# Kernel optimization log

Measured on AMD Instinct MI355X. Metric: run time of the kernel, lower is better.

## Reference

```python
import jax, jax.numpy as jnp
import numpy as np

B, S, IN, H = 64, 1024, 256, 512

def setup_inputs() -> dict:
    key = jax.random.key(0)
    ks = jax.random.split(key, 9)
    inputs = jax.random.normal(ks[0], (B, S, IN), dtype=jnp.float32)
    timestamps = jax.random.uniform(ks[1], (B, S), dtype=jnp.float32)
    input_lens = jax.random.randint(ks[2], (B,), 1, S + 1, dtype=jnp.int64)
    sc_h = 1.0 / np.sqrt(H)
    sc_i = 1.0 / np.sqrt(IN)
    # torch Linear: y = x @ W.T + b; store transposed weights [in, out]
    W_all = jax.random.uniform(ks[3], (H, 4 * H), jnp.float32, -sc_h, sc_h)
    b_all = jax.random.uniform(ks[4], (4 * H,), jnp.float32, -sc_h, sc_h)
    U_all = jax.random.uniform(ks[5], (IN, 4 * H), jnp.float32, -sc_i, sc_i)
    b_u = jax.random.uniform(ks[6], (4 * H,), jnp.float32, -sc_i, sc_i)
    W_d = jax.random.uniform(ks[7], (H, H), jnp.float32, -sc_h, sc_h)
    b_d = jax.random.uniform(ks[8], (H,), jnp.float32, -sc_h, sc_h)
    return {"inputs": inputs, "timestamps": timestamps, "input_lens": input_lens,
            "W_all": W_all, "b_all": b_all, "U_all": U_all, "b_u": b_u,
            "W_d": W_d, "b_d": b_d}

def _time_lstm(inputs, timestamps, input_lens, W_all, b_all, U_all, b_u, W_d, b_d):
    b = inputs.shape[0]
    hdim = W_d.shape[0]
    # precompute input projection once: [B,S,4H]
    x_proj = jnp.einsum('bsi,ig->bsg', inputs, U_all) + b_u
    # elapse gate: 1 / log(e + dt), [B,S,1]
    g = 1.0 / jnp.log(jnp.float32(np.e) + timestamps)

    def step(carry, xs):
        h, c = carry
        x_t, g_t = xs  # [B,4H], [B]
        c_s1 = jnp.tanh(c @ W_d + b_d)
        c_adj = c - c_s1 + c_s1 * g_t[:, None]
        outs = h @ W_all + b_all + x_t
        f, i, o, c_tmp = jnp.split(outs, 4, axis=1)
        c_new = jax.nn.sigmoid(f) * c_adj + jax.nn.sigmoid(i) * jnp.tanh(c_tmp)
        h_new = jax.nn.sigmoid(o) * jnp.tanh(c_new)
        return (h_new, c_new), (h_new, c_new)

    h0 = jnp.zeros((b, hdim), inputs.dtype)
    c0 = jnp.zeros((b, hdim), inputs.dtype)
    xs = (jnp.swapaxes(x_proj, 0, 1), jnp.swapaxes(g, 0, 1))  # time-major
    _, (h_seq, c_seq) = jax.lax.scan(step, (h0, c0), xs)
    h_seq = jnp.swapaxes(h_seq, 0, 1)  # [B,S,H]
    c_seq = jnp.swapaxes(c_seq, 0, 1)

    seq = inputs.shape[1]
    mask = (jnp.arange(seq)[None, :] < input_lens[:, None])  # [B,S]
    outputs = jnp.where(mask[:, :, None], h_seq, 0.0)  # zeros past length, like original
    last_idx = (input_lens - 1)[:, None, None]  # [B,1,1]
    last_h = jnp.take_along_axis(h_seq, jnp.broadcast_to(last_idx, (b, 1, hdim)), axis=1)[:, 0]
    last_c = jnp.take_along_axis(c_seq, jnp.broadcast_to(last_idx, (b, 1, hdim)), axis=1)[:, 0]
    return outputs, last_h, last_c

def reference(inputs, timestamps, input_lens, W_all, b_all, U_all, b_u, W_d, b_d):
    return _time_lstm(inputs, timestamps, input_lens, W_all, b_all, U_all, b_u, W_d, b_d)
```

## Files before the change

kernel.cpp:

```cpp
#include <hip/hip_runtime.h>


typedef _Float16 f16;
typedef _Float16 f16x8 __attribute__((ext_vector_type(8)));
typedef float f32x4 __attribute__((ext_vector_type(4)));

#define S_ 1024
#define IN_ 256
#define H_ 512
#define ECONST 2.718281828459045f

__device__ __forceinline__ float sigf(float x) { return 1.0f / (1.0f + __expf(-x)); }
__device__ __forceinline__ float tanh_f(float x) { return 1.0f - 2.0f / (__expf(2.0f * x) + 1.0f); }

__device__ __forceinline__ unsigned int pack_hc(float h, float c) {
    union { f16 f; unsigned short u; } ph, pc;
    ph.f = (f16)h; pc.f = (f16)c;
    return ((unsigned int)pc.u << 16) | (unsigned int)ph.u;
}

__launch_bounds__(320, 2)
__global__ void tlstm_scan(
    const float* __restrict__ inputs, const float* __restrict__ tstamps,
    const int* __restrict__ lens,
    const float* __restrict__ W_all, const float* __restrict__ b_all,
    const float* __restrict__ U_all, const float* __restrict__ b_u,
    const float* __restrict__ W_d, const float* __restrict__ b_d,
    float* __restrict__ out0, float* __restrict__ out1, float* __restrict__ out2,
    unsigned long long* __restrict__ hcbuf, unsigned int* __restrict__ flags)
{
    __shared__ __align__(16) f16 A_sm[96 * 16 * 8];
    __shared__ __align__(16) f16 C_sm[64 * 16 * 8];
    __shared__ float outs_sm[5 * 16 * 17];
    __shared__ float c_loc[16 * 16];
    __shared__ float bias_sm[5 * 16];
    __shared__ int   len_sm[16];

    const int tid    = threadIdx.x;
    const int grp    = blockIdx.x & 3;
    const int member = blockIdx.x >> 2;
    const int wave   = tid >> 6;
    const int lane   = tid & 63;
    const int q      = lane >> 4;
    const int r16    = lane & 15;
    const int j0     = member * 16;

    f16x8 bw[24];
    if (wave < 4) {
        const int col = wave * 512 + j0 + r16;
#pragma unroll
        for (int kk = 0; kk < 24; ++kk) {
            f16x8 v;
            const int kbase = kk * 32 + q * 8;
#pragma unroll
            for (int e = 0; e < 8; ++e) {
                const int k = kbase + e;
                const float w = (kk < 16) ? W_all[k * 2048 + col]
                                          : U_all[(k - 512) * 2048 + col];
                v[e] = (f16)w;
            }
            bw[kk] = v;
        }
    } else {
        const int col = j0 + r16;
#pragma unroll
        for (int kk = 0; kk < 16; ++kk) {
            f16x8 v;
            const int kbase = kk * 32 + q * 8;
#pragma unroll
            for (int e = 0; e < 8; ++e) v[e] = (f16)W_d[(kbase + e) * 512 + col];
            bw[kk] = v;
        }
#pragma unroll
        for (int kk = 16; kk < 24; ++kk) bw[kk] = bw[0];
    }

    int sl[7];
    int ns = 0;
    for (int s = wave; s < 32; s += 5)
        if (s != member) sl[ns++] = s;

    {
        uint4 z; z.x = z.y = z.z = z.w = 0u;
        uint4* a4 = (uint4*)A_sm;
        uint4* c4 = (uint4*)C_sm;
        for (int i = tid; i < 1024; i += 320) { a4[i] = z; c4[i] = z; }
        if (tid < 256) c_loc[tid] = 0.0f;
        if (tid < 64) {
            const int w = tid >> 4, n = tid & 15;
            const int col = w * 512 + j0 + n;
            bias_sm[w * 16 + n] = b_all[col] + b_u[col];
        } else if (tid < 80) {
            const int n = tid & 15;
            bias_sm[64 + n] = b_d[j0 + n];
        }
        if (tid < 16) len_sm[tid] = lens[grp * 16 + tid];
        for (int idx = tid; idx < 1024; idx += 320) {
            const int b = idx >> 6;
            const int kx0 = (idx & 63) << 2;
            const float4 v = *(const float4*)&inputs[(((size_t)(grp * 16 + b)) * S_ + 0) * IN_ + kx0];
            union { f16 h[4]; uint2 u; } p;
            p.h[0] = (f16)v.x; p.h[1] = (f16)v.y; p.h[2] = (f16)v.z; p.h[3] = (f16)v.w;
            const int kb = 64 + (kx0 >> 3), e = kx0 & 7;
            *(uint2*)&A_sm[(kb * 16 + b) * 8 + e] = p.u;
        }
    }
    __syncthreads();

    unsigned long long* const hc_g = hcbuf + (size_t)grp * 2 * 4096;
    unsigned int* const flg = flags + grp * 32;

    for (int t = 0; t < S_; ++t) {
        float ts = 0.0f;
        if (tid < 256) {
            const int gb = grp * 16 + (tid >> 4);
            ts = tstamps[(size_t)gb * S_ + t];
        }

        f32x4 acc0 = {0.f, 0.f, 0.f, 0.f}, acc1 = {0.f, 0.f, 0.f, 0.f};
        if (wave < 4) {
            const f16* abase = &A_sm[(q * 16 + r16) * 8];
#pragma unroll
            for (int kk = 0; kk < 24; ++kk) {
                const f16x8 a = *(const f16x8*)(abase + kk * 512);
                if (kk & 1) acc1 = __builtin_amdgcn_mfma_f32_16x16x32_f16(a, bw[kk], acc1, 0, 0, 0);
                else        acc0 = __builtin_amdgcn_mfma_f32_16x16x32_f16(a, bw[kk], acc0, 0, 0, 0);
            }
        } else {
            const f16* abase = &C_sm[(q * 16 + r16) * 8];
#pragma unroll
            for (int kk = 0; kk < 16; ++kk) {
                const f16x8 a = *(const f16x8*)(abase + kk * 512);
                if (kk & 1) acc1 = __builtin_amdgcn_mfma_f32_16x16x32_f16(a, bw[kk], acc1, 0, 0, 0);
                else        acc0 = __builtin_amdgcn_mfma_f32_16x16x32_f16(a, bw[kk], acc0, 0, 0, 0);
            }
        }
        const f32x4 acc = acc0 + acc1;
#pragma unroll
        for (int r = 0; r < 4; ++r)
            outs_sm[(wave * 16 + q * 4 + r) * 17 + r16] = acc[r];
        __syncthreads();

        if (tid < 256) {
            const int b = tid >> 4, jj = tid & 15;
            const int gb = grp * 16 + b;
            const float f  = outs_sm[(0 * 16 + b) * 17 + jj] + bias_sm[0  + jj];
            const float i_ = outs_sm[(1 * 16 + b) * 17 + jj] + bias_sm[16 + jj];
            const float o  = outs_sm[(2 * 16 + b) * 17 + jj] + bias_sm[32 + jj];
            const float ct = outs_sm[(3 * 16 + b) * 17 + jj] + bias_sm[48 + jj];
            const float d  = outs_sm[(4 * 16 + b) * 17 + jj] + bias_sm[64 + jj];
            const float gt = 1.0f / __logf(ECONST + ts);
            const float cs1   = tanh_f(d);
            const float cprev = c_loc[tid];
            const float cadj  = cprev - cs1 + cs1 * gt;
            const float cnew  = sigf(f) * cadj + sigf(i_) * tanh_f(ct);
            const float hnew  = sigf(o) * tanh_f(cnew);
            c_loc[tid] = cnew;
            const int col = j0 + jj;
            const int len = len_sm[b];
            out0[((size_t)gb * S_ + t) * H_ + col] = (t < len) ? hnew : 0.0f;
            if (t == len - 1) {
                out1[gb * H_ + col] = hnew;
                out2[gb * H_ + col] = cnew;
            }
            const int fi = ((col >> 3) * 16 + b) * 8 + (col & 7);
            ((f16*)A_sm)[fi] = (f16)hnew;
            ((f16*)C_sm)[fi] = (f16)cnew;
            unsigned int* dw = (unsigned int*)(hc_g + (size_t)(t & 1) * 4096);
            __hip_atomic_store(dw + member * 256 + tid, pack_hc(hnew, cnew),
                               __ATOMIC_RELAXED, __HIP_MEMORY_SCOPE_AGENT);
        }
        __syncthreads();

        if (t < S_ - 1) {
            const unsigned int tag = (unsigned int)(t + 1);
            if (tid == 0)
                __hip_atomic_store(&flg[member], tag,
                                   __ATOMIC_RELAXED, __HIP_MEMORY_SCOPE_AGENT);

            float4 xv[4];
            if (tid < 256) {
#pragma unroll
                for (int k2 = 0; k2 < 4; ++k2) {
                    const int idx = k2 * 256 + tid;
                    const int b = idx >> 6;
                    const int kx0 = (idx & 63) << 2;
                    xv[k2] = *(const float4*)&inputs[(((size_t)(grp * 16 + b)) * S_ + (t + 1)) * IN_ + kx0];
                }
            }

            for (;;) {
                unsigned int fl = tag;
                if (lane < ns)
                    fl = __hip_atomic_load(&flg[sl[lane]],
                                           __ATOMIC_RELAXED, __HIP_MEMORY_SCOPE_AGENT);
                if (__ballot(fl >= tag) == ~0ull) break;
            }

            const unsigned long long* src = hc_g + (size_t)(t & 1) * 4096;
            unsigned long long v[7][2];
#pragma unroll
            for (int u = 0; u < 7; ++u) {
                if (u < ns) {
                    const int s = sl[u];
                    v[u][0] = __hip_atomic_load(src + s * 128 + lane,
                                                __ATOMIC_RELAXED, __HIP_MEMORY_SCOPE_AGENT);
                    v[u][1] = __hip_atomic_load(src + s * 128 + 64 + lane,
                                                __ATOMIC_RELAXED, __HIP_MEMORY_SCOPE_AGENT);
                }
            }
#pragma unroll
            for (int u = 0; u < 7; ++u) {
                if (u < ns) {
                    const int s = sl[u];
#pragma unroll
                    for (int dd = 0; dd < 2; ++dd) {
                        const int j = dd * 64 + lane;
                        const int b = j >> 3;
                        const int colL = (j & 7) * 2;
                        const int col = s * 16 + colL;
                        const unsigned long long qv = v[u][dd];
                        const unsigned int d0 = (unsigned int)qv;
                        const unsigned int d1 = (unsigned int)(qv >> 32);
                        const unsigned int hpair = (d0 & 0xFFFFu) | (d1 << 16);
                        const unsigned int cpair = (d0 >> 16) | (d1 & 0xFFFF0000u);
                        const int fi = ((col >> 3) * 16 + b) * 8 + (col & 7);
                        *(unsigned int*)((f16*)A_sm + fi) = hpair;
                        *(unsigned int*)((f16*)C_sm + fi) = cpair;
                    }
                }
            }

            if (tid < 256) {
#pragma unroll
                for (int k2 = 0; k2 < 4; ++k2) {
                    const int idx = k2 * 256 + tid;
                    const int b = idx >> 6;
                    const int kx0 = (idx & 63) << 2;
                    union { f16 h[4]; uint2 u; } p;
                    p.h[0] = (f16)xv[k2].x; p.h[1] = (f16)xv[k2].y;
                    p.h[2] = (f16)xv[k2].z; p.h[3] = (f16)xv[k2].w;
                    const int kb = 64 + (kx0 >> 3), e = kx0 & 7;
                    *(uint2*)&A_sm[(kb * 16 + b) * 8 + e] = p.u;
                }
            }
            __syncthreads();
        }
    }
}

extern "C" void kernel_launch(void* const* d_in, const int* in_sizes, int n_in,
                              void* d_out, int out_size, void* d_ws, size_t ws_size,
                              hipStream_t stream) {
    const float* inputs  = (const float*)d_in[0];
    const float* tstamps = (const float*)d_in[1];
    const int*   lens    = (const int*)d_in[2];
    const float* W_all   = (const float*)d_in[3];
    const float* b_all   = (const float*)d_in[4];
    const float* U_all   = (const float*)d_in[5];
    const float* b_u     = (const float*)d_in[6];
    const float* W_d     = (const float*)d_in[7];
    const float* b_d     = (const float*)d_in[8];

    float* out0 = (float*)d_out;
    float* out1 = out0 + (size_t)64 * 1024 * 512;
    float* out2 = out1 + (size_t)64 * 512;

    char* ws = (char*)d_ws;
    unsigned int* flags = (unsigned int*)ws;
    unsigned long long* hcbuf = (unsigned long long*)(ws + 1024);

    hipMemsetAsync(ws, 0, 1024, stream);

    tlstm_scan<<<dim3(128), dim3(320), 0, stream>>>(
        inputs, tstamps, lens, W_all, b_all, U_all, b_u, W_d, b_d,
        out0, out1, out2, hcbuf, flags);
}
```

Before: 3.488 ms.

## Replace flag-based barrier with tagged per-element h/c exchange polling

Drops the separate per-block flag array and its store/poll handshake. Each h and c value is now written as a 32-bit word holding the step tag in its upper 16 bits, and consumers poll the data itself until every tag matches. This removes one global round trip and one __syncthreads per step, at the cost of doubling the exchanged bytes and having each of 256 threads poll 64 words. Every block now reads the full buffer, including its own slice, rather than only other members' slices. The memset is removed and launch bounds are relaxed to one block per SM; stale workspace contents could in principle alias a tag.

```diff
diff --git a/kernel.cpp b/kernel.cpp
--- a/kernel.cpp
+++ b/kernel.cpp
@@ -13,13 +13,11 @@
 __device__ __forceinline__ float sigf(float x) { return 1.0f / (1.0f + __expf(-x)); }
 __device__ __forceinline__ float tanh_f(float x) { return 1.0f - 2.0f / (__expf(2.0f * x) + 1.0f); }
 
-__device__ __forceinline__ unsigned int pack_hc(float h, float c) {
-    union { f16 f; unsigned short u; } ph, pc;
-    ph.f = (f16)h; pc.f = (f16)c;
-    return ((unsigned int)pc.u << 16) | (unsigned int)ph.u;
+__device__ __forceinline__ unsigned short f16bits(float x) {
+    union { f16 f; unsigned short u; } p; p.f = (f16)x; return p.u;
 }
 
-__launch_bounds__(320, 2)
+__launch_bounds__(320, 1)
 __global__ void tlstm_scan(
     const float* __restrict__ inputs, const float* __restrict__ tstamps,
     const int* __restrict__ lens,
@@ -27,7 +25,7 @@
     const float* __restrict__ U_all, const float* __restrict__ b_u,
     const float* __restrict__ W_d, const float* __restrict__ b_d,
     float* __restrict__ out0, float* __restrict__ out1, float* __restrict__ out2,
-    unsigned long long* __restrict__ hcbuf, unsigned int* __restrict__ flags)
+    unsigned int* __restrict__ hbuf, unsigned int* __restrict__ cbuf)
 {
     __shared__ __align__(16) f16 A_sm[96 * 16 * 8];
     __shared__ __align__(16) f16 C_sm[64 * 16 * 8];
@@ -74,11 +72,6 @@
 #pragma unroll
         for (int kk = 16; kk < 24; ++kk) bw[kk] = bw[0];
     }
-
-    int sl[7];
-    int ns = 0;
-    for (int s = wave; s < 32; s += 5)
-        if (s != member) sl[ns++] = s;
 
     {
         uint4 z; z.x = z.y = z.z = z.w = 0u;
@@ -91,31 +84,26 @@
             const int col = w * 512 + j0 + n;
             bias_sm[w * 16 + n] = b_all[col] + b_u[col];
         } else if (tid < 80) {
-            const int n = tid & 15;
-            bias_sm[64 + n] = b_d[j0 + n];
+            bias_sm[64 + (tid & 15)] = b_d[j0 + (tid & 15)];
         }
         if (tid < 16) len_sm[tid] = lens[grp * 16 + tid];
         for (int idx = tid; idx < 1024; idx += 320) {
             const int b = idx >> 6;
             const int kx0 = (idx & 63) << 2;
-            const float4 v = *(const float4*)&inputs[(((size_t)(grp * 16 + b)) * S_ + 0) * IN_ + kx0];
+            const float4 v = *(const float4*)&inputs[(((size_t)(grp * 16 + b)) * S_) * IN_ + kx0];
             union { f16 h[4]; uint2 u; } p;
             p.h[0] = (f16)v.x; p.h[1] = (f16)v.y; p.h[2] = (f16)v.z; p.h[3] = (f16)v.w;
-            const int kb = 64 + (kx0 >> 3), e = kx0 & 7;
-            *(uint2*)&A_sm[(kb * 16 + b) * 8 + e] = p.u;
+            *(uint2*)&A_sm[((64 + (kx0 >> 3)) * 16 + b) * 8 + (kx0 & 7)] = p.u;
         }
     }
     __syncthreads();
 
-    unsigned long long* const hc_g = hcbuf + (size_t)grp * 2 * 4096;
-    unsigned int* const flg = flags + grp * 32;
+    unsigned int* const hb_g = hbuf + (size_t)grp * 16384;
+    unsigned int* const cb_g = cbuf + (size_t)grp * 16384;
 
     for (int t = 0; t < S_; ++t) {
         float ts = 0.0f;
-        if (tid < 256) {
-            const int gb = grp * 16 + (tid >> 4);
-            ts = tstamps[(size_t)gb * S_ + t];
-        }
+        if (tid < 256) ts = tstamps[(size_t)(grp * 16 + (tid >> 4)) * S_ + t];
 
         f32x4 acc0 = {0.f, 0.f, 0.f, 0.f}, acc1 = {0.f, 0.f, 0.f, 0.f};
         if (wave < 4) {
@@ -140,6 +128,10 @@
         for (int r = 0; r < 4; ++r)
             outs_sm[(wave * 16 + q * 4 + r) * 17 + r16] = acc[r];
         __syncthreads();
+
+        const unsigned int tag = (unsigned int)(t + 1);
+        unsigned int* const hph = hb_g + (t & 1) * 8192;
+        unsigned int* const cph = cb_g + (t & 1) * 8192;
 
         if (tid < 256) {
             const int b = tid >> 4, jj = tid & 15;
@@ -163,21 +155,16 @@
                 out1[gb * H_ + col] = hnew;
                 out2[gb * H_ + col] = cnew;
             }
-            const int fi = ((col >> 3) * 16 + b) * 8 + (col & 7);
-            ((f16*)A_sm)[fi] = (f16)hnew;
-            ((f16*)C_sm)[fi] = (f16)cnew;
-            unsigned int* dw = (unsigned int*)(hc_g + (size_t)(t & 1) * 4096);
-            __hip_atomic_store(dw + member * 256 + tid, pack_hc(hnew, cnew),
-                               __ATOMIC_RELAXED, __HIP_MEMORY_SCOPE_AGENT);
-        }
-        __syncthreads();
+            if (t < S_ - 1) {
+                const int ci = member * 256 + tid;
+                __hip_atomic_store(hph + ci, (tag << 16) | (unsigned int)f16bits(hnew),
+                                   __ATOMIC_RELAXED, __HIP_MEMORY_SCOPE_AGENT);
+                __hip_atomic_store(cph + ci, (tag << 16) | (unsigned int)f16bits(cnew),
+                                   __ATOMIC_RELAXED, __HIP_MEMORY_SCOPE_AGENT);
+            }
+        }
 
         if (t < S_ - 1) {
-            const unsigned int tag = (unsigned int)(t + 1);
-            if (tid == 0)
-                __hip_atomic_store(&flg[member], tag,
-                                   __ATOMIC_RELAXED, __HIP_MEMORY_SCOPE_AGENT);
-
             float4 xv[4];
             if (tid < 256) {
 #pragma unroll
@@ -185,53 +172,49 @@
                     const int idx = k2 * 256 + tid;
                     const int b = idx >> 6;
                     const int kx0 = (idx & 63) << 2;
-                    xv[k2] = *(const float4*)&inputs[(((size_t)(grp * 16 + b)) * S_ + (t + 1)) * IN_ + kx0];
-                }
-            }
-
-            for (;;) {
-                unsigned int fl = tag;
-                if (lane < ns)
-                    fl = __hip_atomic_load(&flg[sl[lane]],
-                                           __ATOMIC_RELAXED, __HIP_MEMORY_SCOPE_AGENT);
-                if (__ballot(fl >= tag) == ~0ull) break;
-            }
-
-            const unsigned long long* src = hc_g + (size_t)(t & 1) * 4096;
-            unsigned long long v[7][2];
-#pragma unroll
-            for (int u = 0; u < 7; ++u) {
-                if (u < ns) {
-                    const int s = sl[u];
-                    v[u][0] = __hip_atomic_load(src + s * 128 + lane,
-                                                __ATOMIC_RELAXED, __HIP_MEMORY_SCOPE_AGENT);
-                    v[u][1] = __hip_atomic_load(src + s * 128 + 64 + lane,
-                                                __ATOMIC_RELAXED, __HIP_MEMORY_SCOPE_AGENT);
-                }
-            }
-#pragma unroll
-            for (int u = 0; u < 7; ++u) {
-                if (u < ns) {
-                    const int s = sl[u];
-#pragma unroll
-                    for (int dd = 0; dd < 2; ++dd) {
-                        const int j = dd * 64 + lane;
-                        const int b = j >> 3;
-                        const int colL = (j & 7) * 2;
-                        const int col = s * 16 + colL;
-                        const unsigned long long qv = v[u][dd];
-                        const unsigned int d0 = (unsigned int)qv;
-                        const unsigned int d1 = (unsigned int)(qv >> 32);
-                        const unsigned int hpair = (d0 & 0xFFFFu) | (d1 << 16);
-                        const unsigned int cpair = (d0 >> 16) | (d1 & 0xFFFF0000u);
-                        const int fi = ((col >> 3) * 16 + b) * 8 + (col & 7);
-                        *(unsigned int*)((f16*)A_sm + fi) = hpair;
-                        *(unsigned int*)((f16*)C_sm + fi) = cpair;
+                    xv[k2] = *(const float4*)&inputs[(size_t)(grp * 16 + b) * S_ * IN_
+                                                     + (size_t)(t + 1) * IN_ + kx0];
+                }
+            }
+
+            if (tid < 256) {
+                unsigned int hv[8][4], cv[8][4];
+                for (;;) {
+                    bool ok = true;
+#pragma unroll
+                    for (int k = 0; k < 8; ++k) {
+                        const unsigned int* bh = hph + tid * 4 + 1024 * k;
+                        const unsigned int* bc = cph + tid * 4 + 1024 * k;
+#pragma unroll
+                        for (int e = 0; e < 4; ++e) {
+                            hv[k][e] = __hip_atomic_load(bh + e, __ATOMIC_RELAXED, __HIP_MEMORY_SCOPE_AGENT);
+                            cv[k][e] = __hip_atomic_load(bc + e, __ATOMIC_RELAXED, __HIP_MEMORY_SCOPE_AGENT);
+                        }
                     }
-                }
-            }
-
-            if (tid < 256) {
+#pragma unroll
+                    for (int k = 0; k < 8; ++k)
+#pragma unroll
+                        for (int e = 0; e < 4; ++e)
+                            ok = ok & ((hv[k][e] >> 16) == tag) & ((cv[k][e] >> 16) == tag);
+                    if (__ballot(ok) == ~0ull) break;
+                }
+#pragma unroll
+                for (int k = 0; k < 8; ++k) {
+                    const int ci = tid + 256 * k;
+                    const int s  = ci >> 6;
+                    const int qd = ci & 63;
+                    const int b  = qd >> 2;
+                    const int jj0 = (qd & 3) << 2;
+                    const int col = s * 16 + jj0;
+                    const int fi = ((col >> 3) * 16 + b) * 8 + (col & 7);
+                    uint2 hp, cp;
+                    hp.x = (hv[k][0] & 0xFFFFu) | (hv[k][1] << 16);
+                    hp.y = (hv[k][2] & 0xFFFFu) | (hv[k][3] << 16);
+                    cp.x = (cv[k][0] & 0xFFFFu) | (cv[k][1] << 16);
+                    cp.y = (cv[k][2] & 0xFFFFu) | (cv[k][3] << 16);
+                    *(uint2*)((f16*)A_sm + fi) = hp;
+                    *(uint2*)((f16*)C_sm + fi) = cp;
+                }
 #pragma unroll
                 for (int k2 = 0; k2 < 4; ++k2) {
                     const int idx = k2 * 256 + tid;
@@ -240,8 +223,7 @@
                     union { f16 h[4]; uint2 u; } p;
                     p.h[0] = (f16)xv[k2].x; p.h[1] = (f16)xv[k2].y;
                     p.h[2] = (f16)xv[k2].z; p.h[3] = (f16)xv[k2].w;
-                    const int kb = 64 + (kx0 >> 3), e = kx0 & 7;
-                    *(uint2*)&A_sm[(kb * 16 + b) * 8 + e] = p.u;
+                    *(uint2*)&A_sm[((64 + (kx0 >> 3)) * 16 + b) * 8 + (kx0 & 7)] = p.u;
                 }
             }
             __syncthreads();
@@ -267,12 +249,11 @@
     float* out2 = out1 + (size_t)64 * 512;
 
     char* ws = (char*)d_ws;
-    unsigned int* flags = (unsigned int*)ws;
-    unsigned long long* hcbuf = (unsigned long long*)(ws + 1024);
-
-    hipMemsetAsync(ws, 0, 1024, stream);
+    unsigned int* hbuf = (unsigned int*)ws;
+    unsigned int* cbuf = (unsigned int*)(ws + 262144);
+
 
     tlstm_scan<<<dim3(128), dim3(320), 0, stream>>>(
         inputs, tstamps, lens, W_all, b_all, U_all, b_u, W_d, b_d,
-        out0, out1, out2, hcbuf, flags);
+        out0, out1, out2, hbuf, cbuf);
 }
```

New measurement: 8.282 ms. 2.37x slower.
